# Kernel optimization log

Measured on AMD Instinct MI355X. Metric: run time of the kernel, lower is better.

Reference implementation:

```python
import jax, jax.numpy as jnp
import numpy as np

EPS = 1e-8


def setup_inputs() -> dict:
    key = jax.random.key(0)
    k1, k2, k3, k4, k5 = jax.random.split(key, 5)
    N, B, T, D = 8, 2, 2048, 2048
    F = 4 * D
    blocks = jax.random.normal(k1, (N, B, T, D), dtype=jnp.float32)
    partial_block = jax.random.normal(k2, (B, T, D), dtype=jnp.float32)
    proj_w = jax.random.normal(k3, (D,), dtype=jnp.float32) * 0.02
    norm_scale = jnp.ones((D,), dtype=jnp.float32)
    ffn_w1 = jax.random.normal(k4, (D, F), dtype=jnp.float32) * 0.02
    ffn_w2 = jax.random.normal(k5, (F, D), dtype=jnp.float32) * 0.02
    return {
        "blocks": blocks,
        "partial_block": partial_block,
        "proj_w": proj_w,
        "norm_scale": norm_scale,
        "ffn_w1": ffn_w1,
        "ffn_w2": ffn_w2,
    }


def reference(blocks, partial_block, proj_w, norm_scale, ffn_w1, ffn_w2):
    # Stack completed blocks with current partial sum: V [N1, B, T, D]
    V = jnp.concatenate([blocks, partial_block[None]], axis=0)
    # RMSNorm over D (keys)
    rms = jnp.sqrt(jnp.mean(V * V, axis=-1, keepdims=True) + EPS)
    K = norm_scale * V / rms
    # Pseudo-query dot-product logits [N1, B, T], softmax over blocks (axis 0)
    logits = jnp.einsum('nbtd,d->nbt', K, proj_w)
    alpha = jax.nn.softmax(logits, axis=0)
    # Weighted sum of raw values -> new hidden state h [B, T, D]
    h = jnp.einsum('nbt,nbtd->btd', alpha, V)
    # Sublayer: standard FFN (D -> 4D gelu -> D)
    f_out = jax.nn.gelu(h @ ffn_w1) @ ffn_w2
    # layer_number % block_size != 0 branch: accumulate partial sum
    new_partial = partial_block + f_out
    return h, new_partial
```

## Files before the change

### kernel.cpp

```cpp
#include <hip/hip_runtime.h>

typedef unsigned short ushort_t;
typedef __bf16 bf16x8 __attribute__((ext_vector_type(8)));
typedef float f32x4 __attribute__((ext_vector_type(4)));

#define NB 8
#define BB 2
#define TT 2048
#define DD 2048
#define FF 8192
#define MM (BB * TT)
#define BTD ((size_t)BB * TT * DD)

__device__ __forceinline__ unsigned short f2bf(float f) {
  unsigned int u = __float_as_uint(f);
  u += 0x7FFFu + ((u >> 16) & 1u);
  return (unsigned short)(u >> 16);
}

__device__ __forceinline__ float gelu_tanh(float x) {
  float u = 0.7978845608028654f * (x + 0.044715f * x * x * x);
  float e = __expf(2.0f * u);
  float th = 1.0f - 2.0f / (e + 1.0f);
  return 0.5f * x * (1.0f + th);
}

template <int N>
__device__ __forceinline__ void wait_vmcnt() {
  if constexpr (N == 0) asm volatile("s_waitcnt vmcnt(0)" ::: "memory");
  else if constexpr (N == 6) asm volatile("s_waitcnt vmcnt(6)" ::: "memory");
  else if constexpr (N == 8) asm volatile("s_waitcnt vmcnt(8)" ::: "memory");
}

#define ASYNC_COPY16(gp, lp)                                                   \
  __builtin_amdgcn_global_load_lds(                                            \
      (__attribute__((address_space(1))) void*)(gp),                           \
      (__attribute__((address_space(3))) void*)(lp), 16, 0, 0)

__global__ __launch_bounds__(256) void transpose_conv(
    const float* __restrict__ in, ushort_t* __restrict__ out, int R, int C) {
  __shared__ float tile[32][33];
  const int tx = threadIdx.x & 31, ty = threadIdx.x >> 5;
  const int r0 = blockIdx.y * 32, c0 = blockIdx.x * 32;
#pragma unroll
  for (int i = 0; i < 32; i += 8)
    tile[ty + i][tx] = in[(size_t)(r0 + ty + i) * C + (c0 + tx)];
  __syncthreads();
#pragma unroll
  for (int i = 0; i < 32; i += 8)
    out[(size_t)(c0 + ty + i) * R + (r0 + tx)] = f2bf(tile[tx][ty + i]);
}

__global__ __launch_bounds__(256) void attn_fuse(
    const float* __restrict__ blocks, const float* __restrict__ partial,
    const float* __restrict__ proj_w, const float* __restrict__ norm_scale,
    float* __restrict__ h_out, ushort_t* __restrict__ h_bf) {
  const int t = threadIdx.x;
  const int bt = blockIdx.x;
  const size_t rowoff = (size_t)bt * DD;
  const int d0 = t * 4;

  float w[8];
  {
    float4 ns = *(const float4*)(norm_scale + d0);
    float4 pw = *(const float4*)(proj_w + d0);
    w[0] = ns.x * pw.x; w[1] = ns.y * pw.y; w[2] = ns.z * pw.z; w[3] = ns.w * pw.w;
    ns = *(const float4*)(norm_scale + 1024 + d0);
    pw = *(const float4*)(proj_w + 1024 + d0);
    w[4] = ns.x * pw.x; w[5] = ns.y * pw.y; w[6] = ns.z * pw.z; w[7] = ns.w * pw.w;
  }

  float vv[9][8];
  float ss[9], dt[9];
#pragma unroll
  for (int n = 0; n < 9; ++n) {
    const float* rp = (n < 8) ? (blocks + (size_t)n * BTD + rowoff)
                              : (partial + rowoff);
    float4 v0 = *(const float4*)(rp + d0);
    float4 v1 = *(const float4*)(rp + 1024 + d0);
    vv[n][0] = v0.x; vv[n][1] = v0.y; vv[n][2] = v0.z; vv[n][3] = v0.w;
    vv[n][4] = v1.x; vv[n][5] = v1.y; vv[n][6] = v1.z; vv[n][7] = v1.w;
    float a = 0.f, c = 0.f;
#pragma unroll
    for (int j = 0; j < 8; ++j) {
      a += vv[n][j] * vv[n][j];
      c += vv[n][j] * w[j];
    }
    ss[n] = a; dt[n] = c;
  }

  __shared__ float red[2][9][4];
  const int lane = t & 63, wv = t >> 6;
#pragma unroll
  for (int n = 0; n < 9; ++n) {
    float a = ss[n], c = dt[n];
#pragma unroll
    for (int off = 32; off > 0; off >>= 1) {
      a += __shfl_down(a, off, 64);
      c += __shfl_down(c, off, 64);
    }
    if (lane == 0) { red[0][n][wv] = a; red[1][n][wv] = c; }
  }
  __syncthreads();
  __shared__ float logit_s[9];
  if (t < 9) {
    float a = red[0][t][0] + red[0][t][1] + red[0][t][2] + red[0][t][3];
    float c = red[1][t][0] + red[1][t][1] + red[1][t][2] + red[1][t][3];
    logit_s[t] = c * rsqrtf(a * (1.0f / (float)DD) + 1e-8f);
  }
  __syncthreads();

  float lg[9], mx = -1e30f;
#pragma unroll
  for (int n = 0; n < 9; ++n) { lg[n] = logit_s[n]; mx = fmaxf(mx, lg[n]); }
  float den = 0.0f;
#pragma unroll
  for (int n = 0; n < 9; ++n) { lg[n] = __expf(lg[n] - mx); den += lg[n]; }
  const float inv = 1.0f / den;

  float h[8] = {0, 0, 0, 0, 0, 0, 0, 0};
#pragma unroll
  for (int n = 0; n < 9; ++n) {
    const float a = lg[n] * inv;
#pragma unroll
    for (int j = 0; j < 8; ++j) h[j] += a * vv[n][j];
  }

  float4 o0 = {h[0], h[1], h[2], h[3]}, o1 = {h[4], h[5], h[6], h[7]};
  *(float4*)(h_out + rowoff + d0) = o0;
  *(float4*)(h_out + rowoff + 1024 + d0) = o1;
  uint2 p0, p1;
  p0.x = (unsigned)f2bf(h[0]) | ((unsigned)f2bf(h[1]) << 16);
  p0.y = (unsigned)f2bf(h[2]) | ((unsigned)f2bf(h[3]) << 16);
  p1.x = (unsigned)f2bf(h[4]) | ((unsigned)f2bf(h[5]) << 16);
  p1.y = (unsigned)f2bf(h[6]) | ((unsigned)f2bf(h[7]) << 16);
  *(uint2*)(h_bf + rowoff + d0) = p0;
  *(uint2*)(h_bf + rowoff + 1024 + d0) = p1;
}

template <int BN, int SBY, int SBX, int MCX, int EPI>
__global__ __launch_bounds__(256, 1) void gemmP(
    const ushort_t* __restrict__ A, const ushort_t* __restrict__ BT,
    const int K, const int N, ushort_t* __restrict__ Cb,
    const float* __restrict__ addend, float* __restrict__ Cf) {
  constexpr int MFR = 8;
  constexpr int NFR = BN / 32;
  constexpr int AS = 16384;
  constexpr int BS = BN * 64;
  constexpr int RS = AS + BS;
  constexpr int LA = 4;
  constexpr int LBN = BS / 4096;
  constexpr int LT = LA + LBN;

  __shared__ __align__(16) char lds[4 * RS];

  const int t = threadIdx.x;
  const int lane = t & 63, wv = t >> 6;
  const int fr = lane & 15, kslot = lane >> 4;
  const int WRow = (wv >> 1) * 128;
  const int WCol = (wv & 1) * (BN / 2);

  const int wg = blockIdx.x;
  const int xcd = wg & 7, local = wg >> 3;
  const int by = (xcd / MCX) * SBY + local / SBX;
  const int bx = (xcd % MCX) * SBX + local % SBX;
  const int row0 = by * 256, col0 = bx * BN;

  const ushort_t* ga[LA];
  const ushort_t* gb[LBN];
#pragma unroll
  for (int j = 0; j < LA; ++j) {
    const int o = j * 4096 + t * 16;
    const int rp = o >> 7;
    const int iX = (o & 127) ^ ((rp & 7) << 4);
    ga[j] = A + (size_t)(row0 + rp * 2 + (iX >> 6)) * K + ((iX & 63) >> 1);
  }
#pragma unroll
  for (int j = 0; j < LBN; ++j) {
    const int o = j * 4096 + t * 16;
    const int rp = o >> 7;
    const int iX = (o & 127) ^ ((rp & 7) << 4);
    gb[j] = BT + (size_t)(col0 + rp * 2 + (iX >> 6)) * K + ((iX & 63) >> 1);
  }

#define STAGE(QQ, KT)                                                          \
  {                                                                            \
    _Pragma("unroll") for (int j = 0; j < LA; ++j)                             \
      ASYNC_COPY16(ga[j] + (size_t)(KT) * 32,                                  \
                   lds + (QQ)*RS + j * 4096 + t * 16);                         \
    _Pragma("unroll") for (int j = 0; j < LBN; ++j)                            \
      ASYNC_COPY16(gb[j] + (size_t)(KT) * 32,                                  \
                   lds + (QQ)*RS + AS + j * 4096 + t * 16);                    \
  }

  const int arp0 = (WRow + fr) >> 1;
  const int aoff =
      arp0 * 128 + (((((fr & 1) << 6) | (kslot << 4))) ^ ((arp0 & 7) << 4));
  const int brp0 = (WCol + fr) >> 1;
  const int boff = AS + brp0 * 128 +
                   (((((fr & 1) << 6) | (kslot << 4))) ^ ((brp0 & 7) << 4));

  bf16x8 a0[MFR], b0[NFR], a1[MFR], b1[NFR];

#define READF(AX, BX, Lb)                                                      \
  {                                                                            \
    _Pragma("unroll") for (int m = 0; m < MFR; ++m)                            \
      AX[m] = *(const bf16x8*)((Lb) + aoff + m * 1024);                        \
    _Pragma("unroll") for (int n = 0; n < NFR; ++n)                            \
      BX[n] = *(const bf16x8*)((Lb) + boff + n * 1024);                        \
  }

  f32x4 acc[MFR][NFR];
#pragma unroll
  for (int m = 0; m < MFR; ++m)
#pragma unroll
    for (int n = 0; n < NFR; ++n) {
      f32x4 z = {0.f, 0.f, 0.f, 0.f};
      acc[m][n] = z;
    }

#define MFMA_(a, b, c) __builtin_amdgcn_mfma_f32_16x16x32_bf16(a, b, c, 0, 0, 0)

#define INTERVAL(QQ, KT, AC, BC, AN, BNX)                                      \
  {                                                                            \
    if ((KT) + 3 < NT) STAGE(((QQ) + 3) & 3, (KT) + 3);                        \
    if ((KT) + 1 < NT) {                                                       \
      const char* Ln = lds + (((QQ) + 1) & 3) * RS;                            \
      READF(AN, BNX, Ln);                                                      \
    }                                                                          \
    __builtin_amdgcn_s_setprio(1);                                             \
    _Pragma("unroll") for (int m = 0; m < MFR; ++m)                            \
      _Pragma("unroll") for (int n = 0; n < NFR; ++n)                          \
        acc[m][n] = MFMA_(AC[m], BC[n], acc[m][n]);                            \
    __builtin_amdgcn_s_setprio(0);                                             \
    if ((KT) + 3 < NT) wait_vmcnt<LT>(); else wait_vmcnt<0>();                 \
    __builtin_amdgcn_s_barrier();                                              \
  }

  const int NT = K >> 5;

  STAGE(0, 0);
  STAGE(1, 1);
  STAGE(2, 2);
  wait_vmcnt<LT>();
  __builtin_amdgcn_s_barrier();
  READF(a0, b0, (const char*)lds);

  for (int t0 = 0; t0 < NT; t0 += 4) {
    INTERVAL(0, t0 + 0, a0, b0, a1, b1);
    INTERVAL(1, t0 + 1, a1, b1, a0, b0);
    INTERVAL(2, t0 + 2, a0, b0, a1, b1);
    INTERVAL(3, t0 + 3, a1, b1, a0, b0);
  }

  const int r4 = kslot * 4;
#pragma unroll
  for (int m = 0; m < MFR; ++m) {
    const int grow = row0 + WRow + m * 16 + r4;
#pragma unroll
    for (int n = 0; n < NFR; ++n) {
      const int gcol = col0 + WCol + n * 16 + fr;
#pragma unroll
      for (int r = 0; r < 4; ++r) {
        const float v = acc[m][n][r];
        const size_t idx = (size_t)(grow + r) * N + gcol;
        if (EPI == 0) {
          Cb[idx] = f2bf(gelu_tanh(v));
        } else {
          Cf[idx] = v + addend[idx];
        }
      }
    }
  }
#undef INTERVAL
#undef MFMA_
#undef READF
#undef STAGE
}

extern "C" void kernel_launch(void* const* d_in, const int* in_sizes, int n_in,
                              void* d_out, int out_size, void* d_ws,
                              size_t ws_size, hipStream_t stream) {
  const float* blocks = (const float*)d_in[0];
  const float* partial = (const float*)d_in[1];
  const float* proj_w = (const float*)d_in[2];
  const float* norm_scale = (const float*)d_in[3];
  const float* w1 = (const float*)d_in[4];
  const float* w2 = (const float*)d_in[5];

  float* out = (float*)d_out;
  float* h_out = out;
  float* new_partial = out + BTD;

  char* ws = (char*)d_ws;
  ushort_t* h_bf = (ushort_t*)ws;
  ushort_t* w1T = (ushort_t*)(ws + (size_t)16777216);
  ushort_t* w2T = (ushort_t*)(ws + (size_t)16777216 + 33554432);
  ushort_t* act = (ushort_t*)(ws + (size_t)16777216 + 2 * 33554432ull);

  transpose_conv<<<dim3(FF / 32, DD / 32), 256, 0, stream>>>(w1, w1T, DD, FF);
  transpose_conv<<<dim3(DD / 32, FF / 32), 256, 0, stream>>>(w2, w2T, FF, DD);

  attn_fuse<<<MM, 256, 0, stream>>>(blocks, partial, proj_w, norm_scale, h_out,
                                    h_bf);

  gemmP<256, 8, 8, 4, 0><<<512, 256, 0, stream>>>(
      h_bf, w1T, DD, FF, act, nullptr, nullptr);
  gemmP<128, 4, 8, 2, 1><<<256, 256, 0, stream>>>(
      act, w2T, FF, DD, nullptr, partial, new_partial);
}
```

Baseline: 437.9 us.

## Use 8-wave GEMM workgroups with configurable warp grid and vectorize weight transpose

New measurement: 393.0 us. 1.11x faster.

```diff
diff --git a/kernel.cpp b/kernel.cpp
--- a/kernel.cpp
+++ b/kernel.cpp
@@ -28,8 +28,8 @@
 template <int N>
 __device__ __forceinline__ void wait_vmcnt() {
   if constexpr (N == 0) asm volatile("s_waitcnt vmcnt(0)" ::: "memory");
-  else if constexpr (N == 6) asm volatile("s_waitcnt vmcnt(6)" ::: "memory");
-  else if constexpr (N == 8) asm volatile("s_waitcnt vmcnt(8)" ::: "memory");
+  else if constexpr (N == 3) asm volatile("s_waitcnt vmcnt(3)" ::: "memory");
+  else if constexpr (N == 4) asm volatile("s_waitcnt vmcnt(4)" ::: "memory");
 }
 
 #define ASYNC_COPY16(gp, lp)                                                   \
@@ -40,15 +40,21 @@
 __global__ __launch_bounds__(256) void transpose_conv(
     const float* __restrict__ in, ushort_t* __restrict__ out, int R, int C) {
   __shared__ float tile[32][33];
-  const int tx = threadIdx.x & 31, ty = threadIdx.x >> 5;
+  const int tx = threadIdx.x & 7;
+  const int ty = threadIdx.x >> 3;
   const int r0 = blockIdx.y * 32, c0 = blockIdx.x * 32;
-#pragma unroll
-  for (int i = 0; i < 32; i += 8)
-    tile[ty + i][tx] = in[(size_t)(r0 + ty + i) * C + (c0 + tx)];
+  float4 v = *(const float4*)(in + (size_t)(r0 + ty) * C + c0 + tx * 4);
+  tile[ty][tx * 4 + 0] = v.x;
+  tile[ty][tx * 4 + 1] = v.y;
+  tile[ty][tx * 4 + 2] = v.z;
+  tile[ty][tx * 4 + 3] = v.w;
   __syncthreads();
-#pragma unroll
-  for (int i = 0; i < 32; i += 8)
-    out[(size_t)(c0 + ty + i) * R + (r0 + tx)] = f2bf(tile[tx][ty + i]);
+  ushort4 o;
+  o.x = f2bf(tile[tx * 4 + 0][ty]);
+  o.y = f2bf(tile[tx * 4 + 1][ty]);
+  o.z = f2bf(tile[tx * 4 + 2][ty]);
+  o.w = f2bf(tile[tx * 4 + 3][ty]);
+  *(ushort4*)(out + (size_t)(c0 + ty) * R + r0 + tx * 4) = o;
 }
 
 __global__ __launch_bounds__(256) void attn_fuse(
@@ -138,18 +144,18 @@
   *(uint2*)(h_bf + rowoff + 1024 + d0) = p1;
 }
 
-template <int BN, int SBY, int SBX, int MCX, int EPI>
-__global__ __launch_bounds__(256, 1) void gemmP(
+template <int BN, int WM, int WN, int SBY, int SBX, int MCX, int EPI>
+__global__ __launch_bounds__(512, 2) void gemmR(
     const ushort_t* __restrict__ A, const ushort_t* __restrict__ BT,
     const int K, const int N, ushort_t* __restrict__ Cb,
     const float* __restrict__ addend, float* __restrict__ Cf) {
-  constexpr int MFR = 8;
-  constexpr int NFR = BN / 32;
+  constexpr int MFR = 256 / WM / 16;
+  constexpr int NFR = BN / WN / 16;
   constexpr int AS = 16384;
   constexpr int BS = BN * 64;
   constexpr int RS = AS + BS;
-  constexpr int LA = 4;
-  constexpr int LBN = BS / 4096;
+  constexpr int LA = 2;
+  constexpr int LBN = BS / 8192;
   constexpr int LT = LA + LBN;
 
   __shared__ __align__(16) char lds[4 * RS];
@@ -157,8 +163,8 @@
   const int t = threadIdx.x;
   const int lane = t & 63, wv = t >> 6;
   const int fr = lane & 15, kslot = lane >> 4;
-  const int WRow = (wv >> 1) * 128;
-  const int WCol = (wv & 1) * (BN / 2);
+  const int WRow = (wv / WN) * (256 / WM);
+  const int WCol = (wv % WN) * (BN / WN);
 
   const int wg = blockIdx.x;
   const int xcd = wg & 7, local = wg >> 3;
@@ -170,14 +176,14 @@
   const ushort_t* gb[LBN];
 #pragma unroll
   for (int j = 0; j < LA; ++j) {
-    const int o = j * 4096 + t * 16;
+    const int o = j * 8192 + t * 16;
     const int rp = o >> 7;
     const int iX = (o & 127) ^ ((rp & 7) << 4);
     ga[j] = A + (size_t)(row0 + rp * 2 + (iX >> 6)) * K + ((iX & 63) >> 1);
   }
 #pragma unroll
   for (int j = 0; j < LBN; ++j) {
-    const int o = j * 4096 + t * 16;
+    const int o = j * 8192 + t * 16;
     const int rp = o >> 7;
     const int iX = (o & 127) ^ ((rp & 7) << 4);
     gb[j] = BT + (size_t)(col0 + rp * 2 + (iX >> 6)) * K + ((iX & 63) >> 1);
@@ -187,10 +193,10 @@
   {                                                                            \
     _Pragma("unroll") for (int j = 0; j < LA; ++j)                             \
       ASYNC_COPY16(ga[j] + (size_t)(KT) * 32,                                  \
-                   lds + (QQ)*RS + j * 4096 + t * 16);                         \
+                   lds + (QQ)*RS + j * 8192 + t * 16);                         \
     _Pragma("unroll") for (int j = 0; j < LBN; ++j)                            \
       ASYNC_COPY16(gb[j] + (size_t)(KT) * 32,                                  \
-                   lds + (QQ)*RS + AS + j * 4096 + t * 16);                    \
+                   lds + (QQ)*RS + AS + j * 8192 + t * 16);                    \
   }
 
   const int arp0 = (WRow + fr) >> 1;
@@ -304,8 +310,8 @@
   attn_fuse<<<MM, 256, 0, stream>>>(blocks, partial, proj_w, norm_scale, h_out,
                                     h_bf);
 
-  gemmP<256, 8, 8, 4, 0><<<512, 256, 0, stream>>>(
+  gemmR<256, 2, 4, 8, 8, 4, 0><<<512, 512, 0, stream>>>(
       h_bf, w1T, DD, FF, act, nullptr, nullptr);
-  gemmP<128, 4, 8, 2, 1><<<256, 256, 0, stream>>>(
+  gemmR<128, 4, 2, 4, 8, 2, 1><<<256, 512, 0, stream>>>(
       act, w2T, FF, DD, nullptr, partial, new_partial);
 }
```
